# Kernel tuning notes

Hardware: AMD Instinct MI355X
Metric: run time of the kernel (lower is better)

Reference implementation:

```python
import jax, jax.numpy as jnp
import numpy as np

GAMMA = 0.01
INFER_STEP = 5


def softor(x, axis, gamma=GAMMA):
    # gamma * logsumexp(x / gamma) along `axis`, rescaled by global max if it exceeds 1
    y = gamma * jax.nn.logsumexp(x / gamma, axis=axis)
    mx = jnp.max(y)
    return jnp.where(mx > 1.0, y / mx, y)


def setup_inputs() -> dict:
    key = jax.random.key(0)
    k1, k2, k3 = jax.random.split(key, 3)
    B, G, C, S, L, m = 32, 2048, 16, 8, 3, 16
    x = jax.random.uniform(k1, (B, G), dtype=jnp.float32)          # valuation vector in [0,1]
    W = jax.random.normal(k2, (m, C), dtype=jnp.float32)           # clause-assignment weights
    I = jax.random.randint(k3, (C, G, S, L), 0, G)                 # index tensor into atom axis
    return {"x": x, "W": W, "I": I}


def reference(x, W, I):
    # x: [B,G] valuations; W: [m,C]; I: [C,G,S,L] int indices into G
    def r(V):
        # all C clause functions at once: gather V along atom axis using I
        gathered = V[:, I]                      # [B,C,G,S,L]
        body = jnp.prod(gathered, axis=-1)      # conjunction over body literals -> [B,C,G,S]
        Cv = softor(body, axis=-1)              # softor over substitutions -> [B,C,G]
        Ws = jax.nn.softmax(W, axis=1)          # [m,C]
        H = jnp.einsum('mc,bcg->mbg', Ws, Cv)   # weighted clause mix -> [m,B,G]
        return softor(H, axis=0)                # softor over m heads -> [B,G]

    R = x
    for _ in range(INFER_STEP):
        R = softor(jnp.stack([R, r(R)], axis=1), axis=1)  # amalgamate old and new facts
    return R
```

## Files before the change

kernel.cpp:

```cpp
#include <hip/hip_runtime.h>

#define GAMMA 0.01f
#define INV_GAMMA 100.0f
#define B 32
#define G 2048
#define C 16
#define S 8
#define L 3
#define M 16
#define NGT 8
#define NCG 2

__device__ __forceinline__ float waveMax(float v) {
#pragma unroll
    for (int off = 32; off > 0; off >>= 1)
        v = fmaxf(v, __shfl_xor(v, off, 64));
    return v;
}

__device__ __forceinline__ float blockMaxBcast(float v, float* scratch) {
    float wm = waveMax(v);
    __syncthreads();
    if ((threadIdx.x & 63) == 0) scratch[threadIdx.x >> 6] = wm;
    __syncthreads();
    return fmaxf(fmaxf(scratch[0], scratch[1]), fmaxf(scratch[2], scratch[3]));
}

__global__ void kinit(const float* __restrict__ W, float* __restrict__ Ws) {
    int t = threadIdx.x;
    int m = t >> 4, c = t & 15;
    float rmax = -INFINITY;
#pragma unroll
    for (int j = 0; j < C; j++) rmax = fmaxf(rmax, W[m * C + j]);
    float rsum = 0.f;
#pragma unroll
    for (int j = 0; j < C; j++) rsum += __expf(W[m * C + j] - rmax);
    Ws[m * C + c] = __expf(W[m * C + c] - rmax) / rsum;
}

__global__ __launch_bounds__(256) void k1(
    const float* __restrict__ Vsrc, const float* __restrict__ Pm3prev,
    const int* __restrict__ I, float* __restrict__ Cv, float* __restrict__ Pm1) {
    __shared__ float Vrow[G];
    __shared__ float scratch[4];
    const int b = blockIdx.z, cg = blockIdx.y, gt = blockIdx.x;
    const int t = threadIdx.x;

    float s = 1.0f;
    if (Pm3prev) {
        float m3 = blockMaxBcast(Pm3prev[t], scratch);
        s = (m3 > 1.0f) ? 1.0f / m3 : 1.0f;
    }

    const float4* V4 = (const float4*)(Vsrc + (size_t)b * G);
    float4* Vr4 = (float4*)Vrow;
#pragma unroll
    for (int j = 0; j < 2; j++) {
        float4 v = V4[t + j * 256];
        v.x *= s; v.y *= s; v.z *= s; v.w *= s;
        Vr4[t + j * 256] = v;
    }
    __syncthreads();

    const int g = gt * 256 + t;
    float ymax = -INFINITY;
#pragma unroll 2
    for (int j = 0; j < 8; j++) {
        const int c = cg * 8 + j;
        const int4* ip = (const int4*)(I + ((size_t)c * G + g) * (S * L));
        int idx[S * L];
#pragma unroll
        for (int q = 0; q < 6; q++) {
            int4 v = ip[q];
            idx[q * 4 + 0] = v.x; idx[q * 4 + 1] = v.y;
            idx[q * 4 + 2] = v.z; idx[q * 4 + 3] = v.w;
        }
        float body[S];
#pragma unroll
        for (int ss = 0; ss < S; ss++)
            body[ss] = Vrow[idx[ss * 3]] * Vrow[idx[ss * 3 + 1]] * Vrow[idx[ss * 3 + 2]];
        float bm = body[0];
#pragma unroll
        for (int ss = 1; ss < S; ss++) bm = fmaxf(bm, body[ss]);
        float sum = 0.f;
#pragma unroll
        for (int ss = 0; ss < S; ss++) sum += __expf((body[ss] - bm) * INV_GAMMA);
        float y = bm + GAMMA * __logf(sum);
        Cv[((size_t)b * C + c) * G + g] = y;
        ymax = fmaxf(ymax, y);
    }

    float wm = waveMax(ymax);
    __syncthreads();
    if ((t & 63) == 0) scratch[t >> 6] = wm;
    __syncthreads();
    if (t == 0)
        Pm1[(b * NCG + cg) * NGT + gt] =
            fmaxf(fmaxf(scratch[0], scratch[1]), fmaxf(scratch[2], scratch[3]));
}

__global__ __launch_bounds__(256) void k2(
    const float* __restrict__ Cv, const float* __restrict__ Ws,
    const float* __restrict__ Pm1, float* __restrict__ Hy, float* __restrict__ Pm2) {
    __shared__ float WsL[M * C];
    __shared__ float scratch[4];
    const int b = blockIdx.y, gt = blockIdx.x, t = threadIdx.x;

    WsL[t] = Ws[t];
    float m1 = blockMaxBcast(fmaxf(Pm1[t], Pm1[t + 256]), scratch);
    float s1 = (m1 > 1.0f) ? 1.0f / m1 : 1.0f;

    const int g = gt * 256 + t;
    float cv[C];
#pragma unroll
    for (int c = 0; c < C; c++)
        cv[c] = s1 * Cv[((size_t)b * C + c) * G + g];

    float h[M];
    float hm = -INFINITY;
#pragma unroll
    for (int m = 0; m < M; m++) {
        float acc = 0.f;
#pragma unroll
        for (int c = 0; c < C; c++) acc = fmaf(WsL[m * C + c], cv[c], acc);
        h[m] = acc; hm = fmaxf(hm, acc);
    }
    float sum = 0.f;
#pragma unroll
    for (int m = 0; m < M; m++) sum += __expf((h[m] - hm) * INV_GAMMA);
    float y = hm + GAMMA * __logf(sum);
    Hy[(size_t)b * G + g] = y;

    float wm = waveMax(y);
    __syncthreads();
    if ((t & 63) == 0) scratch[t >> 6] = wm;
    __syncthreads();
    if (t == 0)
        Pm2[b * NGT + gt] =
            fmaxf(fmaxf(scratch[0], scratch[1]), fmaxf(scratch[2], scratch[3]));
}

__global__ __launch_bounds__(256) void k3(
    const float* __restrict__ Rprev, const float* __restrict__ Pm3prev,
    const float* __restrict__ Hy, const float* __restrict__ Pm2,
    float* __restrict__ Ry, float* __restrict__ Pm3) {
    __shared__ float scratch[4];
    const int t = threadIdx.x;
    const int i = blockIdx.x * 256 + t;

    float sp = 1.0f;
    if (Pm3prev) {
        float m = blockMaxBcast(Pm3prev[t], scratch);
        sp = (m > 1.0f) ? 1.0f / m : 1.0f;
    }
    float m2 = blockMaxBcast(Pm2[t], scratch);
    float s2 = (m2 > 1.0f) ? 1.0f / m2 : 1.0f;

    float Rv = sp * Rprev[i];
    float rv = s2 * Hy[i];
    float a = fmaxf(Rv, rv), d = fminf(Rv, rv);
    float y = a + GAMMA * __logf(1.0f + __expf((d - a) * INV_GAMMA));
    Ry[i] = y;

    float wm = waveMax(y);
    __syncthreads();
    if ((t & 63) == 0) scratch[t >> 6] = wm;
    __syncthreads();
    if (t == 0)
        Pm3[blockIdx.x] =
            fmaxf(fmaxf(scratch[0], scratch[1]), fmaxf(scratch[2], scratch[3]));
}

__global__ void kout(const float* __restrict__ Ry, const float* __restrict__ Pm3,
                     float* __restrict__ out) {
    __shared__ float scratch[4];
    const int t = threadIdx.x;
    const int i = blockIdx.x * 256 + t;
    float m = blockMaxBcast(Pm3[t], scratch);
    float s = (m > 1.0f) ? 1.0f / m : 1.0f;
    out[i] = s * Ry[i];
}

extern "C" void kernel_launch(void* const* d_in, const int* in_sizes, int n_in,
                              void* d_out, int out_size, void* d_ws, size_t ws_size,
                              hipStream_t stream) {
    const float* x = (const float*)d_in[0];
    const float* W = (const float*)d_in[1];
    const int*   I = (const int*)d_in[2];
    float* out = (float*)d_out;

    float* ws   = (float*)d_ws;
    float* Ws   = ws;
    float* Pm1  = ws + 256;
    float* Pm2  = Pm1 + 5 * 512;
    float* Pm3  = Pm2 + 5 * 256;
    float* Cv   = Pm3 + 5 * 256;
    float* Hy   = Cv + (size_t)B * C * G;
    float* Ry   = Hy + (size_t)B * G;

    kinit<<<1, 256, 0, stream>>>(W, Ws);

    const float* V = x;
    const float* p3prev = nullptr;
    for (int it = 0; it < 5; it++) {
        float* pm1 = Pm1 + it * 512;
        float* pm2 = Pm2 + it * 256;
        float* pm3 = Pm3 + it * 256;
        k1<<<dim3(NGT, NCG, B), 256, 0, stream>>>(V, p3prev, I, Cv, pm1);
        k2<<<dim3(NGT, B), 256, 0, stream>>>(Cv, Ws, pm1, Hy, pm2);
        k3<<<dim3((B * G) / 256), 256, 0, stream>>>(V, p3prev, Hy, pm2, Ry, pm3);
        V = Ry;
        p3prev = pm3;
    }
    kout<<<(B * G) / 256, 256, 0, stream>>>(Ry, Pm3 + 4 * 256, out);
}
```

Before: 142.1 us.

## Pack gather indices as 16-bit byte offsets and batch four rows per LDS gather

A new init kernel converts the int32 index tensor into a transposed, coalesced uint16 array of pre-scaled byte offsets. The clause kernel then loads four batch rows interleaved in shared memory and gathers a float4 per index, so each index fetch serves four batches. Grid and block shapes are reworked around this layout, and the exp/log calls switch to exp2/log2 with folded constants. The point is to cut index-tensor traffic and the number of LDS gather instructions, at the cost of a one-time packing pass each call and a larger shared-memory footprint per block.

```diff
diff --git a/kernel.cpp b/kernel.cpp
--- a/kernel.cpp
+++ b/kernel.cpp
@@ -1,15 +1,16 @@
 #include <hip/hip_runtime.h>
 
 #define GAMMA 0.01f
-#define INV_GAMMA 100.0f
 #define B 32
 #define G 2048
 #define C 16
 #define S 8
 #define L 3
 #define M 16
-#define NGT 8
-#define NCG 2
+#define Q 24
+
+#define K_EXP 144.26950408889634f
+#define K_LOG 0.006931471805599453f
 
 __device__ __forceinline__ float waveMax(float v) {
 #pragma unroll
@@ -26,77 +27,133 @@
     return fmaxf(fmaxf(scratch[0], scratch[1]), fmaxf(scratch[2], scratch[3]));
 }
 
-__global__ void kinit(const float* __restrict__ W, float* __restrict__ Ws) {
-    int t = threadIdx.x;
-    int m = t >> 4, c = t & 15;
-    float rmax = -INFINITY;
-#pragma unroll
-    for (int j = 0; j < C; j++) rmax = fmaxf(rmax, W[m * C + j]);
-    float rsum = 0.f;
-#pragma unroll
-    for (int j = 0; j < C; j++) rsum += __expf(W[m * C + j] - rmax);
-    Ws[m * C + c] = __expf(W[m * C + c] - rmax) / rsum;
-}
-
-__global__ __launch_bounds__(256) void k1(
+__device__ __forceinline__ float blockMaxBcast8(float v, float* scratch) {
+    float wm = waveMax(v);
+    __syncthreads();
+    if ((threadIdx.x & 63) == 0) scratch[threadIdx.x >> 6] = wm;
+    __syncthreads();
+    float r = scratch[0];
+#pragma unroll
+    for (int j = 1; j < 8; j++) r = fmaxf(r, scratch[j]);
+    return r;
+}
+
+__global__ __launch_bounds__(256) void kinit(
+    const float* __restrict__ W, const int* __restrict__ I,
+    float* __restrict__ Ws, unsigned short* __restrict__ Ipk) {
+    const int t = blockIdx.x * 256 + threadIdx.x;
+    const int c = t >> 11, g = t & 2047;
+    const int4* ip4 = (const int4*)(I + ((size_t)c * G + g) * Q);
+    int idx[Q];
+#pragma unroll
+    for (int j = 0; j < 6; j++) {
+        int4 v = ip4[j];
+        idx[4 * j + 0] = v.x; idx[4 * j + 1] = v.y;
+        idx[4 * j + 2] = v.z; idx[4 * j + 3] = v.w;
+    }
+#pragma unroll
+    for (int q = 0; q < Q; q++)
+        Ipk[((size_t)c * Q + q) * G + g] = (unsigned short)(idx[q] << 4);
+
+    if (blockIdx.x == 0) {
+        const int m = threadIdx.x >> 4, cc = threadIdx.x & 15;
+        float rmax = -INFINITY;
+#pragma unroll
+        for (int j = 0; j < C; j++) rmax = fmaxf(rmax, W[m * C + j]);
+        float rsum = 0.f;
+#pragma unroll
+        for (int j = 0; j < C; j++) rsum += __expf(W[m * C + j] - rmax);
+        Ws[m * C + cc] = __expf(W[m * C + cc] - rmax) / rsum;
+    }
+}
+
+__global__ __launch_bounds__(512) void k1(
     const float* __restrict__ Vsrc, const float* __restrict__ Pm3prev,
-    const int* __restrict__ I, float* __restrict__ Cv, float* __restrict__ Pm1) {
-    __shared__ float Vrow[G];
-    __shared__ float scratch[4];
-    const int b = blockIdx.z, cg = blockIdx.y, gt = blockIdx.x;
+    const unsigned short* __restrict__ Ipk,
+    float* __restrict__ Cv, float* __restrict__ Pm1) {
+    __shared__ __align__(16) float V4[G * 4];
+    __shared__ float scratch[8];
     const int t = threadIdx.x;
+    const int gt = blockIdx.x, cg = blockIdx.y, bq = blockIdx.z;
+    const int b0 = bq * 4;
 
     float s = 1.0f;
     if (Pm3prev) {
-        float m3 = blockMaxBcast(Pm3prev[t], scratch);
+        float m3 = blockMaxBcast8(Pm3prev[t & 255], scratch);
         s = (m3 > 1.0f) ? 1.0f / m3 : 1.0f;
     }
 
-    const float4* V4 = (const float4*)(Vsrc + (size_t)b * G);
-    float4* Vr4 = (float4*)Vrow;
-#pragma unroll
-    for (int j = 0; j < 2; j++) {
-        float4 v = V4[t + j * 256];
-        v.x *= s; v.y *= s; v.z *= s; v.w *= s;
-        Vr4[t + j * 256] = v;
-    }
-    __syncthreads();
-
-    const int g = gt * 256 + t;
+    {
+        const int bb = t & 3, gb = t >> 2;
+        const float* src = Vsrc + (size_t)(b0 + bb) * G;
+#pragma unroll
+        for (int k = 0; k < 16; k++) {
+            const int g = gb + (k << 7);
+            V4[(g << 2) + bb] = s * src[g];
+        }
+    }
+    __syncthreads();
+
+    const int g = (gt << 7) + (t & 127);
+    const int cbase = cg * 8 + (t >> 7) * 2;
+    const char* vb = (const char*)V4;
     float ymax = -INFINITY;
-#pragma unroll 2
-    for (int j = 0; j < 8; j++) {
-        const int c = cg * 8 + j;
-        const int4* ip = (const int4*)(I + ((size_t)c * G + g) * (S * L));
-        int idx[S * L];
-#pragma unroll
-        for (int q = 0; q < 6; q++) {
-            int4 v = ip[q];
-            idx[q * 4 + 0] = v.x; idx[q * 4 + 1] = v.y;
-            idx[q * 4 + 2] = v.z; idx[q * 4 + 3] = v.w;
-        }
-        float body[S];
-#pragma unroll
-        for (int ss = 0; ss < S; ss++)
-            body[ss] = Vrow[idx[ss * 3]] * Vrow[idx[ss * 3 + 1]] * Vrow[idx[ss * 3 + 2]];
-        float bm = body[0];
-#pragma unroll
-        for (int ss = 1; ss < S; ss++) bm = fmaxf(bm, body[ss]);
-        float sum = 0.f;
-#pragma unroll
-        for (int ss = 0; ss < S; ss++) sum += __expf((body[ss] - bm) * INV_GAMMA);
-        float y = bm + GAMMA * __logf(sum);
-        Cv[((size_t)b * C + c) * G + g] = y;
-        ymax = fmaxf(ymax, y);
+
+#pragma unroll
+    for (int cc = 0; cc < 2; cc++) {
+        const int c = cbase + cc;
+        const unsigned short* ip = Ipk + (size_t)c * Q * G + g;
+        unsigned int off[Q];
+#pragma unroll
+        for (int q = 0; q < Q; q++) off[q] = ip[(size_t)q * G];
+
+        float4 body[S];
+#pragma unroll
+        for (int ss = 0; ss < S; ss++) {
+            float4 v0 = *(const float4*)(vb + off[ss * 3 + 0]);
+            float4 v1 = *(const float4*)(vb + off[ss * 3 + 1]);
+            float4 v2 = *(const float4*)(vb + off[ss * 3 + 2]);
+            body[ss] = make_float4(v0.x * v1.x * v2.x, v0.y * v1.y * v2.y,
+                                   v0.z * v1.z * v2.z, v0.w * v1.w * v2.w);
+        }
+        float4 bm = body[0];
+#pragma unroll
+        for (int ss = 1; ss < S; ss++) {
+            bm.x = fmaxf(bm.x, body[ss].x); bm.y = fmaxf(bm.y, body[ss].y);
+            bm.z = fmaxf(bm.z, body[ss].z); bm.w = fmaxf(bm.w, body[ss].w);
+        }
+        float4 sum = make_float4(0.f, 0.f, 0.f, 0.f);
+#pragma unroll
+        for (int ss = 0; ss < S; ss++) {
+            sum.x += exp2f((body[ss].x - bm.x) * K_EXP);
+            sum.y += exp2f((body[ss].y - bm.y) * K_EXP);
+            sum.z += exp2f((body[ss].z - bm.z) * K_EXP);
+            sum.w += exp2f((body[ss].w - bm.w) * K_EXP);
+        }
+        float4 y;
+        y.x = fmaf(K_LOG, log2f(sum.x), bm.x);
+        y.y = fmaf(K_LOG, log2f(sum.y), bm.y);
+        y.z = fmaf(K_LOG, log2f(sum.z), bm.z);
+        y.w = fmaf(K_LOG, log2f(sum.w), bm.w);
+
+        const size_t cgo = (size_t)c * G + g;
+        Cv[(size_t)(b0 + 0) * (C * G) + cgo] = y.x;
+        Cv[(size_t)(b0 + 1) * (C * G) + cgo] = y.y;
+        Cv[(size_t)(b0 + 2) * (C * G) + cgo] = y.z;
+        Cv[(size_t)(b0 + 3) * (C * G) + cgo] = y.w;
+        ymax = fmaxf(ymax, fmaxf(fmaxf(y.x, y.y), fmaxf(y.z, y.w)));
     }
 
     float wm = waveMax(ymax);
     __syncthreads();
     if ((t & 63) == 0) scratch[t >> 6] = wm;
     __syncthreads();
-    if (t == 0)
-        Pm1[(b * NCG + cg) * NGT + gt] =
-            fmaxf(fmaxf(scratch[0], scratch[1]), fmaxf(scratch[2], scratch[3]));
+    if (t == 0) {
+        float r = scratch[0];
+#pragma unroll
+        for (int j = 1; j < 8; j++) r = fmaxf(r, scratch[j]);
+        Pm1[(bq * 2 + cg) * 16 + gt] = r;
+    }
 }
 
 __global__ __launch_bounds__(256) void k2(
@@ -107,7 +164,7 @@
     const int b = blockIdx.y, gt = blockIdx.x, t = threadIdx.x;
 
     WsL[t] = Ws[t];
-    float m1 = blockMaxBcast(fmaxf(Pm1[t], Pm1[t + 256]), scratch);
+    float m1 = blockMaxBcast(Pm1[t], scratch);
     float s1 = (m1 > 1.0f) ? 1.0f / m1 : 1.0f;
 
     const int g = gt * 256 + t;
@@ -127,8 +184,8 @@
     }
     float sum = 0.f;
 #pragma unroll
-    for (int m = 0; m < M; m++) sum += __expf((h[m] - hm) * INV_GAMMA);
-    float y = hm + GAMMA * __logf(sum);
+    for (int m = 0; m < M; m++) sum += exp2f((h[m] - hm) * K_EXP);
+    float y = fmaf(K_LOG, log2f(sum), hm);
     Hy[(size_t)b * G + g] = y;
 
     float wm = waveMax(y);
@@ -136,7 +193,7 @@
     if ((t & 63) == 0) scratch[t >> 6] = wm;
     __syncthreads();
     if (t == 0)
-        Pm2[b * NGT + gt] =
+        Pm2[b * 8 + gt] =
             fmaxf(fmaxf(scratch[0], scratch[1]), fmaxf(scratch[2], scratch[3]));
 }
 
@@ -159,7 +216,7 @@
     float Rv = sp * Rprev[i];
     float rv = s2 * Hy[i];
     float a = fmaxf(Rv, rv), d = fminf(Rv, rv);
-    float y = a + GAMMA * __logf(1.0f + __expf((d - a) * INV_GAMMA));
+    float y = fmaf(K_LOG, log2f(1.0f + exp2f((d - a) * K_EXP)), a);
     Ry[i] = y;
 
     float wm = waveMax(y);
@@ -171,8 +228,9 @@
             fmaxf(fmaxf(scratch[0], scratch[1]), fmaxf(scratch[2], scratch[3]));
 }
 
-__global__ void kout(const float* __restrict__ Ry, const float* __restrict__ Pm3,
-                     float* __restrict__ out) {
+__global__ __launch_bounds__(256) void kout(
+    const float* __restrict__ Ry, const float* __restrict__ Pm3,
+    float* __restrict__ out) {
     __shared__ float scratch[4];
     const int t = threadIdx.x;
     const int i = blockIdx.x * 256 + t;
@@ -189,25 +247,26 @@
     const int*   I = (const int*)d_in[2];
     float* out = (float*)d_out;
 
-    float* ws   = (float*)d_ws;
-    float* Ws   = ws;
-    float* Pm1  = ws + 256;
-    float* Pm2  = Pm1 + 5 * 512;
-    float* Pm3  = Pm2 + 5 * 256;
-    float* Cv   = Pm3 + 5 * 256;
-    float* Hy   = Cv + (size_t)B * C * G;
-    float* Ry   = Hy + (size_t)B * G;
-
-    kinit<<<1, 256, 0, stream>>>(W, Ws);
+    float* ws  = (float*)d_ws;
+    float* Ws  = ws;
+    float* Pm1 = Ws + 256;
+    float* Pm2 = Pm1 + 5 * 256;
+    float* Pm3 = Pm2 + 5 * 256;
+    float* Cv  = Pm3 + 5 * 256;
+    float* Hy  = Cv + (size_t)B * C * G;
+    float* Ry  = Hy + (size_t)B * G;
+    unsigned short* Ipk = (unsigned short*)(Ry + (size_t)B * G);
+
+    kinit<<<dim3(C * G / 256), 256, 0, stream>>>(W, I, Ws, Ipk);
 
     const float* V = x;
     const float* p3prev = nullptr;
     for (int it = 0; it < 5; it++) {
-        float* pm1 = Pm1 + it * 512;
+        float* pm1 = Pm1 + it * 256;
         float* pm2 = Pm2 + it * 256;
         float* pm3 = Pm3 + it * 256;
-        k1<<<dim3(NGT, NCG, B), 256, 0, stream>>>(V, p3prev, I, Cv, pm1);
-        k2<<<dim3(NGT, B), 256, 0, stream>>>(Cv, Ws, pm1, Hy, pm2);
+        k1<<<dim3(16, 2, 8), 512, 0, stream>>>(V, p3prev, Ipk, Cv, pm1);
+        k2<<<dim3(8, B), 256, 0, stream>>>(Cv, Ws, pm1, Hy, pm2);
         k3<<<dim3((B * G) / 256), 256, 0, stream>>>(V, p3prev, Hy, pm2, Ry, pm3);
         V = Ry;
         p3prev = pm3;
```

Result: slower. 145.5 us (+2.4%).
